# Kernel optimization log

Hardware: AMD Instinct MI355X
Metric: run time of the kernel (lower is better)

The kernel has to match this reference:

```python
import jax, jax.numpy as jnp
import numpy as np

N, CIN, T, V, COUT = 64, 64, 256, 25, 128
CI = COUT // 2  # inter_channels
EPS = 1e-5


def setup_inputs() -> dict:
    key = jax.random.key(0)
    ks = jax.random.split(key, 12)
    s = 0.05
    d = {}
    d['x'] = jax.random.normal(ks[0], (N, CIN, T, V), jnp.float32)
    d['A'] = jax.random.normal(ks[1], (3, V, V), jnp.float32) * s
    d['Al'] = jax.random.normal(ks[2], (3, V, V), jnp.float32) * s
    d['Wp'] = jax.random.normal(ks[3], (3, COUT, CIN), jnp.float32) * s
    d['bp'] = jnp.zeros((3, COUT), jnp.float32)
    d['Wm1'] = jax.random.normal(ks[4], (CI, CIN), jnp.float32) * s
    d['bm1'] = jnp.zeros((CI,), jnp.float32)
    d['Wm2'] = jax.random.normal(ks[5], (CI, CIN), jnp.float32) * s
    d['bm2'] = jnp.zeros((CI,), jnp.float32)
    d['Wm3'] = jax.random.normal(ks[6], (COUT, CI), jnp.float32) * s
    d['bm3'] = jnp.zeros((COUT,), jnp.float32)
    d['Wm4'] = jax.random.normal(ks[7], (COUT, CIN), jnp.float32) * s
    d['bm4'] = jnp.zeros((COUT,), jnp.float32)
    d['alpha'] = jax.random.normal(ks[8], (1,), jnp.float32) * s
    d['bn_gamma'] = jnp.ones((COUT,), jnp.float32)
    d['bn_beta'] = jnp.zeros((COUT,), jnp.float32)
    d['down_W'] = jax.random.normal(ks[9], (COUT, CIN), jnp.float32) * s
    d['down_gamma'] = jnp.ones((COUT,), jnp.float32)
    d['down_beta'] = jnp.zeros((COUT,), jnp.float32)
    return d


def _bn_train(y, gamma, beta):
    # BatchNorm2d training forward: biased batch stats over (N, T, V)
    mu = jnp.mean(y, axis=(0, 2, 3), keepdims=True)
    var = jnp.var(y, axis=(0, 2, 3), keepdims=True)
    return (y - mu) * jax.lax.rsqrt(var + EPS) * gamma[None, :, None, None] + beta[None, :, None, None]


def reference(x, A, Al, Wp, bp, Wm1, bm1, Wm2, bm2, Wm3, bm3, Wm4, bm4,
              alpha, bn_gamma, bn_beta, down_W, down_gamma, down_beta):
    Tn = x.shape[2]
    # --- static graph branch: sum over 3 subsets of (A+Al) graph matmuls ---
    Xp = jnp.einsum('soi,nitv->snotv', Wp, x) + bp[:, None, :, None, None]  # (3,N,COUT,T,V)
    y = jnp.einsum('suv,snctv->nctu', A + Al, Xp)                           # (N,COUT,T,V)
    # --- dynamic adjacency from temporal-difference features ---
    xf = jnp.mean(jnp.einsum('oi,nitv->notv', Wm1, x[:, :, :Tn - 2]) + bm1[None, :, None, None], axis=2)  # (N,CI,V)
    xb = jnp.mean(jnp.einsum('oi,nitv->notv', Wm2, x[:, :, 2:]) + bm2[None, :, None, None], axis=2)       # (N,CI,V)
    diff = xb[:, :, :, None] - xf[:, :, None, :]                            # (N,CI,V,V)
    Rd = jnp.tanh(jnp.einsum('oi,nivw->novw', Wm3, diff) + bm3[None, :, None, None])  # (N,COUT,V,V)
    Xm = jnp.einsum('oi,nitv->notv', Wm4, x) + bm4[None, :, None, None]     # (N,COUT,T,V)
    z = jnp.einsum('ncuv,nctv->nctu', Rd, Xm)                               # (N,COUT,T,V)
    y = z * alpha + y
    # --- BN, residual (1x1 conv + BN down-path since CIN != COUT), ReLU ---
    y = _bn_train(y, bn_gamma, bn_beta)
    d = jnp.einsum('oi,nitv->notv', down_W, x)  # no bias
    d = _bn_train(d, down_gamma, down_beta)
    return jax.nn.relu(y + d)
```

## Files before the change

kernel.cpp:

```cpp
#include <hip/hip_runtime.h>
#include <stdint.h>

typedef unsigned short u16;
typedef unsigned int   u32;
typedef short bf16x8 __attribute__((ext_vector_type(8)));
typedef float f32x4  __attribute__((ext_vector_type(4)));

#define N_    64
#define CIN_  64
#define T_    256
#define V_    25
#define COUT_ 128
#define CI_   64
#define EPS_  1e-5f
#define CNT_  409600.0f

#define MFMA16(a,b,c) __builtin_amdgcn_mfma_f32_16x16x32_bf16((a),(b),(c),0,0,0)

__device__ __forceinline__ u16 f2bf(float f) {
  u32 u = __float_as_uint(f);
  u += 0x7fffu + ((u >> 16) & 1u);
  return (u16)(u >> 16);
}
__device__ __forceinline__ float bf2f(u16 h) { return __uint_as_float(((u32)h) << 16); }

__global__ __launch_bounds__(256) void k_pack(const float* __restrict__ Wp, const float* __restrict__ Wm4,
                                              const float* __restrict__ dW, const float* __restrict__ A,
                                              const float* __restrict__ Al,
                                              u16* __restrict__ w5, u16* __restrict__ bst) {
  int tid = threadIdx.x;
  for (int i = tid; i < 640 * 64; i += 256) {
    int r = i >> 6, k = i & 63;
    float v = (r < 384) ? Wp[i] : (r < 512) ? Wm4[(r - 384) * 64 + k] : dW[(r - 512) * 64 + k];
    w5[i] = f2bf(v);
  }
  for (int i = tid; i < 3 * 32 * 32; i += 256) {
    int s = i >> 10, rem = i & 1023, u = rem >> 5, v = rem & 31;
    float val = (u < 25 && v < 25) ? (A[(s * 25 + u) * 25 + v] + Al[(s * 25 + u) * 25 + v]) : 0.f;
    bst[i] = f2bf(val);
  }
}

__global__ __launch_bounds__(256) void k_means(const float* __restrict__ x,
                                               float* __restrict__ mf, float* __restrict__ mb) {
  int i = blockIdx.x, n = blockIdx.y;
  const float* src = x + ((size_t)n * CIN_ + i) * T_ * V_;
  __shared__ float xs[T_ * V_];
  __shared__ float pf[8][32], pb[8][32];
  for (int idx = threadIdx.x; idx < T_ * V_; idx += 256) xs[idx] = src[idx];
  __syncthreads();
  int v = threadIdx.x & 31, g = threadIdx.x >> 5;
  float sf = 0.f, sb = 0.f;
  if (v < V_) {
    for (int t = g; t < T_; t += 8) {
      float val = xs[t * V_ + v];
      if (t < T_ - 2) sf += val;
      if (t >= 2)     sb += val;
    }
  }
  pf[g][v] = sf; pb[g][v] = sb;
  __syncthreads();
  if (threadIdx.x < V_) {
    float af = 0.f, ab = 0.f;
    for (int gg = 0; gg < 8; gg++) { af += pf[gg][threadIdx.x]; ab += pb[gg][threadIdx.x]; }
    size_t o = ((size_t)n * CIN_ + i) * V_ + threadIdx.x;
    mf[o] = af * (1.0f / 254.0f);
    mb[o] = ab * (1.0f / 254.0f);
  }
}

__global__ __launch_bounds__(256) void k_rd(
    const float* __restrict__ mf, const float* __restrict__ mb,
    const float* __restrict__ Wm1, const float* __restrict__ bm1,
    const float* __restrict__ Wm2, const float* __restrict__ bm2,
    const float* __restrict__ Wm3, const float* __restrict__ bm3,
    const float* __restrict__ bm4, const float* __restrict__ alpha,
    const float* __restrict__ A, const float* __restrict__ Al, const float* __restrict__ bp,
    u16* __restrict__ rdws, float* __restrict__ biasws) {
  int n = blockIdx.x;
  int tid = threadIdx.x;
  __shared__ float MfL[CIN_][V_], MbL[CIN_][V_], xfL[CI_][V_], xbL[CI_][V_];
  __shared__ float PL[COUT_ * V_], QL[COUT_ * V_], rsumL[3][V_];
  for (int idx = tid; idx < CIN_ * V_; idx += 256) {
    MfL[idx / V_][idx % V_] = mf[(size_t)n * CIN_ * V_ + idx];
    MbL[idx / V_][idx % V_] = mb[(size_t)n * CIN_ * V_ + idx];
  }
  if (tid < 75) {
    int s = tid / 25, u = tid % 25;
    float acc = 0.f;
    for (int v = 0; v < 25; v++) acc += A[(s * 25 + u) * 25 + v] + Al[(s * 25 + u) * 25 + v];
    rsumL[s][u] = acc;
  }
  __syncthreads();
  for (int idx = tid; idx < CI_ * V_; idx += 256) {
    int o = idx / V_, v = idx % V_;
    float af = bm1[o], ab = bm2[o];
    for (int i = 0; i < CIN_; i++) {
      af += Wm1[o * CIN_ + i] * MfL[i][v];
      ab += Wm2[o * CIN_ + i] * MbL[i][v];
    }
    xfL[o][v] = af; xbL[o][v] = ab;
  }
  __syncthreads();
  for (int idx = tid; idx < COUT_ * V_; idx += 256) {
    int c = idx / V_, u = idx % V_;
    float p = 0.f, q = 0.f;
    for (int i = 0; i < CI_; i++) {
      p += Wm3[c * CI_ + i] * xbL[i][u];
      q += Wm3[c * CI_ + i] * xfL[i][u];
    }
    PL[idx] = p; QL[idx] = q;
  }
  __syncthreads();
  float al = alpha[0];
  for (int r = tid; r < COUT_ * V_; r += 256) {
    int c = r / V_, u = r % V_;
    float pv = PL[r] + bm3[c];
    float acc = 0.f;
    u16* dst = rdws + ((size_t)(n * COUT_ + c) * 25 + u) * 32;
    for (int w = 0; w < 25; w++) {
      float val = al * tanhf(pv - QL[c * V_ + w]);
      dst[w] = f2bf(val);
      acc += val;
    }
    for (int w = 25; w < 32; w++) dst[w] = 0;
    float yb = 0.f;
    for (int s = 0; s < 3; s++) yb += bp[s * COUT_ + c] * rsumL[s][u];
    biasws[(size_t)(n * COUT_ + c) * 25 + u] = bm4[c] * acc + yb;
  }
}

__global__ __launch_bounds__(256, 2) void k_main(
    const float* __restrict__ x, const u16* __restrict__ w5, const u16* __restrict__ bst,
    const u16* __restrict__ rdws, const float* __restrict__ biasws,
    u16* __restrict__ out16, float* __restrict__ partials) {
  __shared__ __align__(16) char smem[59904];
  __shared__ float statsL[512];
  const int tid = threadIdx.x;
  const int w = tid >> 6, l = tid & 63;
  const int lc = l & 15, lq = l >> 4;
  const int n = blockIdx.y, tc = blockIdx.x, t0 = tc * 16;

  {
    u32* xslw = (u32*)smem;
    const float* xb = x + (size_t)n * CIN_ * T_ * V_ + (size_t)t0 * V_;
    for (int idx = tid; idx < 32 * 416; idx += 256) {
      int i2 = idx / 416, p = idx - i2 * 416;
      float a = 0.f, b = 0.f;
      if (p < 400) {
        a = xb[(size_t)(2 * i2)     * (T_ * V_) + p];
        b = xb[(size_t)(2 * i2 + 1) * (T_ * V_) + p];
      }
      xslw[p * 36 + i2] = ((u32)f2bf(b) << 16) | (u32)f2bf(a);
    }
  }
  bf16x8 bw[3][2];
  #pragma unroll
  for (int s = 0; s < 3; s++)
    #pragma unroll
    for (int ut = 0; ut < 2; ut++)
      bw[s][ut] = *(const bf16x8*)(bst + (s * 32 + ut * 16 + lc) * 32 + lq * 8);
  __syncthreads();

  bf16x8 xf[7][2] = {};
  #pragma unroll
  for (int pi = 0; pi < 7; pi++) {
    int pt = w + pi * 4;
    if (pt < 26) {
      #pragma unroll
      for (int ks = 0; ks < 2; ks++)
        xf[pi][ks] = *(const bf16x8*)((const u16*)smem + (pt * 16 + lc) * 72 + ks * 32 + lq * 8);
    }
  }
  __syncthreads();

  {
    uint4 z4 = {0, 0, 0, 0};
    uint4* q = (uint4*)smem;
    for (int idx = tid; idx < 2304; idx += 256) q[idx] = z4;
    statsL[tid] = 0.f; statsL[tid + 256] = 0.f;
  }
  __syncthreads();

  u16* xpl = (u16*)smem;
  const f32x4 zz = {0.f, 0.f, 0.f, 0.f};

  for (int g = 0; g < 8; g++) {
    const int c0 = g * 16;
    f32x4 acc[4][2];
    #pragma unroll
    for (int cl = 0; cl < 4; cl++) { acc[cl][0] = zz; acc[cl][1] = zz; }
    float ds[4] = {0.f, 0.f, 0.f, 0.f}, dq[4] = {0.f, 0.f, 0.f, 0.f};

    #pragma unroll
    for (int h = 0; h < 2; h++) {
      const int nsl = h ? 3 : 2;
      bf16x8 af[3][2];
      #pragma unroll
      for (int si = 0; si < 3; si++) if (si < nsl) {
        int sl = h * 2 + si;
        #pragma unroll
        for (int ks = 0; ks < 2; ks++)
          af[si][ks] = *(const bf16x8*)(w5 + ((sl * 128 + c0 + lc) * 64 + ks * 32 + lq * 8));
      }
      #pragma unroll
      for (int pi = 0; pi < 7; pi++) {
        int pt = w + pi * 4;
        if (pt >= 26) continue;
        f32x4 pa[3];
        #pragma unroll
        for (int si = 0; si < 3; si++) if (si < nsl) {
          pa[si] = MFMA16(af[si][0], xf[pi][0], zz);
          pa[si] = MFMA16(af[si][1], xf[pi][1], pa[si]);
        }
        int p = pt * 16 + lc;
        if (p < 400) {
          u32 up = (u32)p, t = up / 25u, v = up - t * 25u;
          #pragma unroll
          for (int si = 0; si < 3; si++) if (si < nsl) {
            int sl = h * 2 + si;
            if (sl < 4) {
              int slot = sl & 1;
              u16* dst = xpl + (4 * lq) * 1152 + t * 72 + slot * 32 + v;
              #pragma unroll
              for (int r = 0; r < 4; r++) dst[r * 1152] = f2bf(pa[si][r]);
            } else {
              size_t ob = (((size_t)(n * COUT_ + c0 + 4 * lq) * T_ + t0 + t) * V_ + v) * 2 + 1;
              #pragma unroll
              for (int r = 0; r < 4; r++) {
                float dv = pa[si][r];
                out16[ob + (size_t)r * (T_ * V_ * 2)] = f2bf(dv);
                ds[r] += dv; dq[r] += dv * dv;
              }
            }
          }
        }
      }
      if (h == 1) {
        #pragma unroll
        for (int r = 0; r < 4; r++) {
          float a = ds[r], b = dq[r];
          #pragma unroll
          for (int off = 1; off < 16; off <<= 1) { a += __shfl_xor(a, off); b += __shfl_xor(b, off); }
          if (lc == 0) {
            atomicAdd(&statsL[(c0 + 4 * lq + r) * 4 + 2], a);
            atomicAdd(&statsL[(c0 + 4 * lq + r) * 4 + 3], b);
          }
        }
      }
      __syncthreads();

      {
        bf16x8 rdf0[4], rdf1[4];
        if (h == 1) {
          #pragma unroll
          for (int cl = 0; cl < 4; cl++) {
            size_t rb = (size_t)(n * COUT_ + c0 + w * 4 + cl) * 25;
            rdf0[cl] = *(const bf16x8*)(rdws + (rb + lc) * 32 + lq * 8);
            int u1c = (lc + 16 < 25) ? lc + 16 : 24;
            rdf1[cl] = *(const bf16x8*)(rdws + (rb + u1c) * 32 + lq * 8);
          }
        }
        #pragma unroll
        for (int cl = 0; cl < 4; cl++) {
          int clocal = w * 4 + cl;
          #pragma unroll
          for (int kl = 0; kl < 2; kl++) {
            bf16x8 aX = *(const bf16x8*)(xpl + clocal * 1152 + lc * 72 + kl * 32 + lq * 8);
            int kk = h * 2 + kl;
            bf16x8 b0, b1;
            if (kk < 3) { b0 = bw[kk][0]; b1 = bw[kk][1]; }
            else        { b0 = rdf0[cl];  b1 = rdf1[cl]; }
            acc[cl][0] = MFMA16(aX, b0, acc[cl][0]);
            acc[cl][1] = MFMA16(aX, b1, acc[cl][1]);
          }
        }
      }
      if (h == 1) {
        #pragma unroll
        for (int cl = 0; cl < 4; cl++) {
          int c = c0 + w * 4 + cl;
          size_t bb = (size_t)(n * COUT_ + c) * 25;
          float bias0 = biasws[bb + lc];
          int u1 = lc + 16; bool v1 = u1 < 25;
          float bias1 = biasws[bb + (v1 ? u1 : 24)];
          size_t ob = ((size_t)(n * COUT_ + c) * T_ + t0) * V_;
          float sy = 0.f, sq = 0.f;
          #pragma unroll
          for (int r = 0; r < 4; r++) {
            int t = 4 * lq + r;
            float y0 = acc[cl][0][r] + bias0;
            out16[(ob + t * 25 + lc) * 2] = f2bf(y0);
            sy += y0; sq += y0 * y0;
            float y1 = acc[cl][1][r] + bias1;
            if (v1) {
              out16[(ob + t * 25 + u1) * 2] = f2bf(y1);
              sy += y1; sq += y1 * y1;
            }
          }
          #pragma unroll
          for (int off = 1; off < 64; off <<= 1) { sy += __shfl_xor(sy, off); sq += __shfl_xor(sq, off); }
          if (l == 0) { atomicAdd(&statsL[c * 4 + 0], sy); atomicAdd(&statsL[c * 4 + 1], sq); }
        }
      }
      __syncthreads();
    }
  }
  int bflat = blockIdx.y * 16 + blockIdx.x;
  for (int j = tid; j < 512; j += 256) partials[(size_t)j * 1024 + bflat] = statsL[j];
}

__global__ __launch_bounds__(256) void k_stats1(const float* __restrict__ partials, float* __restrict__ colsum) {
  int w = threadIdx.x >> 6, l = threadIdx.x & 63;
  for (int ci = 0; ci < 8; ci++) {
    int j = blockIdx.x * 32 + w * 8 + ci;
    float s = 0.f;
    for (int it = 0; it < 16; it++) s += partials[(size_t)j * 1024 + it * 64 + l];
    #pragma unroll
    for (int off = 1; off < 64; off <<= 1) s += __shfl_xor(s, off);
    if (l == 0) colsum[j] = s;
  }
}

__global__ __launch_bounds__(128) void k_stats2(
    const float* __restrict__ colsum,
    const float* __restrict__ bn_g, const float* __restrict__ bn_b,
    const float* __restrict__ dn_g, const float* __restrict__ dn_b,
    float* __restrict__ params) {
  int c = threadIdx.x;
  float sy = colsum[c * 4], syy = colsum[c * 4 + 1], sd = colsum[c * 4 + 2], sdd = colsum[c * 4 + 3];
  float muY = sy / CNT_, varY = syy / CNT_ - muY * muY;
  float muD = sd / CNT_, varD = sdd / CNT_ - muD * muD;
  float sY = bn_g[c] * rsqrtf(varY + EPS_);
  float sD = dn_g[c] * rsqrtf(varD + EPS_);
  float off = bn_b[c] - muY * sY + dn_b[c] - muD * sD;
  params[c * 4 + 0] = sY; params[c * 4 + 1] = sD; params[c * 4 + 2] = off;
}

__global__ __launch_bounds__(256) void k_final(u32* __restrict__ io, const float* __restrict__ params) {
  int slab = blockIdx.x;
  int c = slab & (COUT_ - 1);
  float sY = params[c * 4], sD = params[c * 4 + 1], off = params[c * 4 + 2];
  size_t base = (size_t)slab * (T_ * V_);
  #pragma unroll 5
  for (int j = 0; j < 25; j++) {
    size_t idx = base + j * 256 + threadIdx.x;
    u32 w = io[idx];
    float y = bf2f((u16)(w & 0xffffu));
    float d = bf2f((u16)(w >> 16));
    float val = fmaf(y, sY, fmaf(d, sD, off));
    io[idx] = __float_as_uint(fmaxf(val, 0.0f));
  }
}

extern "C" void kernel_launch(void* const* d_in, const int* in_sizes, int n_in,
                              void* d_out, int out_size, void* d_ws, size_t ws_size,
                              hipStream_t stream) {
  const float* x    = (const float*)d_in[0];
  const float* A    = (const float*)d_in[1];
  const float* Al   = (const float*)d_in[2];
  const float* Wp   = (const float*)d_in[3];
  const float* bp   = (const float*)d_in[4];
  const float* Wm1  = (const float*)d_in[5];
  const float* bm1  = (const float*)d_in[6];
  const float* Wm2  = (const float*)d_in[7];
  const float* bm2  = (const float*)d_in[8];
  const float* Wm3  = (const float*)d_in[9];
  const float* bm3  = (const float*)d_in[10];
  const float* Wm4  = (const float*)d_in[11];
  const float* bm4  = (const float*)d_in[12];
  const float* alpha= (const float*)d_in[13];
  const float* bn_g = (const float*)d_in[14];
  const float* bn_b = (const float*)d_in[15];
  const float* dW   = (const float*)d_in[16];
  const float* dn_g = (const float*)d_in[17];
  const float* dn_b = (const float*)d_in[18];

  char* ws = (char*)d_ws;
  float* mf       = (float*)(ws + 0);
  float* mb       = (float*)(ws + 409600);
  u16*   rdws     = (u16*)  (ws + 819200);
  float* biasws   = (float*)(ws + 13926400);
  u16*   w5       = (u16*)  (ws + 14745600);
  u16*   bstw     = (u16*)  (ws + 14827520);
  float* partials = (float*)(ws + 14833664);
  float* colsum   = (float*)(ws + 16930816);
  float* params   = (float*)(ws + 16932864);

  k_pack <<<dim3(1),       dim3(256), 0, stream>>>(Wp, Wm4, dW, A, Al, w5, bstw);
  k_means<<<dim3(64, 64),  dim3(256), 0, stream>>>(x, mf, mb);
  k_rd   <<<dim3(64),      dim3(256), 0, stream>>>(mf, mb, Wm1, bm1, Wm2, bm2, Wm3, bm3,
                                                   bm4, alpha, A, Al, bp, rdws, biasws);
  k_main <<<dim3(16, 64),  dim3(256), 0, stream>>>(x, w5, bstw, rdws, biasws,
                                                   (u16*)d_out, partials);
  k_stats1<<<dim3(16),     dim3(256), 0, stream>>>(partials, colsum);
  k_stats2<<<dim3(1),      dim3(128), 0, stream>>>(colsum, bn_g, bn_b, dn_g, dn_b, params);
  k_final<<<dim3(64 * 128),dim3(256), 0, stream>>>((u32*)d_out, params);
}
```

Baseline: 681.7 us.

## Split Rd kernel for parallelism, shrink main LDS for occupancy, vectorize loads

Splits the per-sample Rd kernel into a projection kernel and a tanh/bias kernel launched over 8x64 blocks, so the costly tanh loop runs across far more blocks. The main kernel stages x in two smaller swizzled LDS halves, which cuts shared memory use and raises launch bounds to 4 blocks per CU. The means and final normalization kernels switch to float4/uint4 vector accesses, and the adjacency row sums move into the pack kernel. Reusing the partials and colsum workspace regions as scratch relies on launch ordering, and the extra sync in the staging loop adds some latency.

Result: slower. 876.6 us (+28.6%).

```diff
diff --git a/kernel.cpp b/kernel.cpp
--- a/kernel.cpp
+++ b/kernel.cpp
@@ -27,7 +27,8 @@
 __global__ __launch_bounds__(256) void k_pack(const float* __restrict__ Wp, const float* __restrict__ Wm4,
                                               const float* __restrict__ dW, const float* __restrict__ A,
                                               const float* __restrict__ Al,
-                                              u16* __restrict__ w5, u16* __restrict__ bst) {
+                                              u16* __restrict__ w5, u16* __restrict__ bst,
+                                              float* __restrict__ rsumw) {
   int tid = threadIdx.x;
   for (int i = tid; i < 640 * 64; i += 256) {
     int r = i >> 6, k = i & 63;
@@ -38,6 +39,12 @@
     int s = i >> 10, rem = i & 1023, u = rem >> 5, v = rem & 31;
     float val = (u < 25 && v < 25) ? (A[(s * 25 + u) * 25 + v] + Al[(s * 25 + u) * 25 + v]) : 0.f;
     bst[i] = f2bf(val);
+  }
+  if (tid < 75) {
+    int s = tid / 25, u = tid % 25;
+    float acc = 0.f;
+    for (int v = 0; v < 25; v++) acc += A[(s * 25 + u) * 25 + v] + Al[(s * 25 + u) * 25 + v];
+    rsumw[tid] = acc;
   }
 }
 
@@ -47,7 +54,11 @@
   const float* src = x + ((size_t)n * CIN_ + i) * T_ * V_;
   __shared__ float xs[T_ * V_];
   __shared__ float pf[8][32], pb[8][32];
-  for (int idx = threadIdx.x; idx < T_ * V_; idx += 256) xs[idx] = src[idx];
+  {
+    float4* xs4 = (float4*)xs;
+    const float4* src4 = (const float4*)src;
+    for (int idx = threadIdx.x; idx < (T_ * V_) / 4; idx += 256) xs4[idx] = src4[idx];
+  }
   __syncthreads();
   int v = threadIdx.x & 31, g = threadIdx.x >> 5;
   float sf = 0.f, sb = 0.f;
@@ -69,27 +80,16 @@
   }
 }
 
-__global__ __launch_bounds__(256) void k_rd(
+__global__ __launch_bounds__(256) void k_rd1(
     const float* __restrict__ mf, const float* __restrict__ mb,
     const float* __restrict__ Wm1, const float* __restrict__ bm1,
     const float* __restrict__ Wm2, const float* __restrict__ bm2,
-    const float* __restrict__ Wm3, const float* __restrict__ bm3,
-    const float* __restrict__ bm4, const float* __restrict__ alpha,
-    const float* __restrict__ A, const float* __restrict__ Al, const float* __restrict__ bp,
-    u16* __restrict__ rdws, float* __restrict__ biasws) {
-  int n = blockIdx.x;
-  int tid = threadIdx.x;
+    const float* __restrict__ Wm3, float* __restrict__ pqws) {
+  int n = blockIdx.x, tid = threadIdx.x;
   __shared__ float MfL[CIN_][V_], MbL[CIN_][V_], xfL[CI_][V_], xbL[CI_][V_];
-  __shared__ float PL[COUT_ * V_], QL[COUT_ * V_], rsumL[3][V_];
   for (int idx = tid; idx < CIN_ * V_; idx += 256) {
     MfL[idx / V_][idx % V_] = mf[(size_t)n * CIN_ * V_ + idx];
     MbL[idx / V_][idx % V_] = mb[(size_t)n * CIN_ * V_ + idx];
-  }
-  if (tid < 75) {
-    int s = tid / 25, u = tid % 25;
-    float acc = 0.f;
-    for (int v = 0; v < 25; v++) acc += A[(s * 25 + u) * 25 + v] + Al[(s * 25 + u) * 25 + v];
-    rsumL[s][u] = acc;
   }
   __syncthreads();
   for (int idx = tid; idx < CI_ * V_; idx += 256) {
@@ -109,70 +109,89 @@
       p += Wm3[c * CI_ + i] * xbL[i][u];
       q += Wm3[c * CI_ + i] * xfL[i][u];
     }
-    PL[idx] = p; QL[idx] = q;
-  }
+    pqws[(size_t)n * 6400 + idx] = p;
+    pqws[(size_t)n * 6400 + 3200 + idx] = q;
+  }
+}
+
+__global__ __launch_bounds__(256) void k_rd2(
+    const float* __restrict__ pqws, const float* __restrict__ rsumw,
+    const float* __restrict__ bm3, const float* __restrict__ bm4,
+    const float* __restrict__ bp, const float* __restrict__ alpha,
+    u16* __restrict__ rdws, float* __restrict__ biasws) {
+  int cg = blockIdx.x, n = blockIdx.y;
+  int c0 = cg * 16, tid = threadIdx.x;
+  __shared__ float Ps[400], Qs[400], rs[75];
+  for (int idx = tid; idx < 400; idx += 256) {
+    Ps[idx] = pqws[(size_t)n * 6400 + c0 * 25 + idx];
+    Qs[idx] = pqws[(size_t)n * 6400 + 3200 + c0 * 25 + idx];
+  }
+  if (tid < 75) rs[tid] = rsumw[tid];
   __syncthreads();
   float al = alpha[0];
-  for (int r = tid; r < COUT_ * V_; r += 256) {
-    int c = r / V_, u = r % V_;
-    float pv = PL[r] + bm3[c];
+  for (int r = tid; r < 400; r += 256) {
+    int cl = r / 25, u = r - cl * 25, c = c0 + cl;
+    float pv = Ps[r] + bm3[c];
     float acc = 0.f;
     u16* dst = rdws + ((size_t)(n * COUT_ + c) * 25 + u) * 32;
-    for (int w = 0; w < 25; w++) {
-      float val = al * tanhf(pv - QL[c * V_ + w]);
-      dst[w] = f2bf(val);
+    for (int w0 = 0; w0 < 25; w0++) {
+      float val = al * tanhf(pv - Qs[cl * 25 + w0]);
+      dst[w0] = f2bf(val);
       acc += val;
     }
-    for (int w = 25; w < 32; w++) dst[w] = 0;
+    for (int w0 = 25; w0 < 32; w0++) dst[w0] = 0;
     float yb = 0.f;
-    for (int s = 0; s < 3; s++) yb += bp[s * COUT_ + c] * rsumL[s][u];
+    for (int s = 0; s < 3; s++) yb += bp[s * COUT_ + c] * rs[s * 25 + u];
     biasws[(size_t)(n * COUT_ + c) * 25 + u] = bm4[c] * acc + yb;
   }
 }
 
-__global__ __launch_bounds__(256, 2) void k_main(
+__global__ __launch_bounds__(256, 4) void k_main(
     const float* __restrict__ x, const u16* __restrict__ w5, const u16* __restrict__ bst,
     const u16* __restrict__ rdws, const float* __restrict__ biasws,
     u16* __restrict__ out16, float* __restrict__ partials) {
-  __shared__ __align__(16) char smem[59904];
+  __shared__ __align__(16) char smem[36864];
   __shared__ float statsL[512];
   const int tid = threadIdx.x;
   const int w = tid >> 6, l = tid & 63;
   const int lc = l & 15, lq = l >> 4;
   const int n = blockIdx.y, tc = blockIdx.x, t0 = tc * 16;
 
-  {
-    u32* xslw = (u32*)smem;
-    const float* xb = x + (size_t)n * CIN_ * T_ * V_ + (size_t)t0 * V_;
-    for (int idx = tid; idx < 32 * 416; idx += 256) {
-      int i2 = idx / 416, p = idx - i2 * 416;
-      float a = 0.f, b = 0.f;
-      if (p < 400) {
-        a = xb[(size_t)(2 * i2)     * (T_ * V_) + p];
-        b = xb[(size_t)(2 * i2 + 1) * (T_ * V_) + p];
-      }
-      xslw[p * 36 + i2] = ((u32)f2bf(b) << 16) | (u32)f2bf(a);
-    }
-  }
   bf16x8 bw[3][2];
   #pragma unroll
   for (int s = 0; s < 3; s++)
     #pragma unroll
     for (int ut = 0; ut < 2; ut++)
       bw[s][ut] = *(const bf16x8*)(bst + (s * 32 + ut * 16 + lc) * 32 + lq * 8);
-  __syncthreads();
 
   bf16x8 xf[7][2] = {};
+  const float* xb = x + (size_t)n * CIN_ * T_ * V_ + (size_t)t0 * V_;
   #pragma unroll
-  for (int pi = 0; pi < 7; pi++) {
-    int pt = w + pi * 4;
-    if (pt < 26) {
-      #pragma unroll
-      for (int ks = 0; ks < 2; ks++)
-        xf[pi][ks] = *(const bf16x8*)((const u16*)smem + (pt * 16 + lc) * 72 + ks * 32 + lq * 8);
-    }
-  }
-  __syncthreads();
+  for (int ks = 0; ks < 2; ks++) {
+    u32* xslw = (u32*)smem;
+    for (int idx = tid; idx < 16 * 416; idx += 256) {
+      int i2 = idx / 416, p = idx - i2 * 416;
+      float a = 0.f, b = 0.f;
+      int ch = ks * 32 + 2 * i2;
+      if (p < 400) {
+        a = xb[(size_t)ch       * (T_ * V_) + p];
+        b = xb[(size_t)(ch + 1) * (T_ * V_) + p];
+      }
+      int f = (p ^ (p >> 2)) & 3;
+      xslw[p * 16 + (i2 ^ (f << 2))] = ((u32)f2bf(b) << 16) | (u32)f2bf(a);
+    }
+    __syncthreads();
+    #pragma unroll
+    for (int pi = 0; pi < 7; pi++) {
+      int pt = w + pi * 4;
+      if (pt < 26) {
+        int p = pt * 16 + lc;
+        int f = (p ^ (p >> 2)) & 3;
+        xf[pi][ks] = *(const bf16x8*)((const u16*)smem + p * 32 + ((lq ^ f) << 3));
+      }
+    }
+    __syncthreads();
+  }
 
   {
     uint4 z4 = {0, 0, 0, 0};
@@ -341,15 +360,19 @@
   int slab = blockIdx.x;
   int c = slab & (COUT_ - 1);
   float sY = params[c * 4], sD = params[c * 4 + 1], off = params[c * 4 + 2];
-  size_t base = (size_t)slab * (T_ * V_);
-  #pragma unroll 5
-  for (int j = 0; j < 25; j++) {
-    size_t idx = base + j * 256 + threadIdx.x;
-    u32 w = io[idx];
-    float y = bf2f((u16)(w & 0xffffu));
-    float d = bf2f((u16)(w >> 16));
-    float val = fmaf(y, sY, fmaf(d, sD, off));
-    io[idx] = __float_as_uint(fmaxf(val, 0.0f));
+  uint4* io4 = (uint4*)io + (size_t)slab * 1600;
+  #pragma unroll
+  for (int j = 0; j < 7; j++) {
+    int idx = j * 256 + (int)threadIdx.x;
+    if (idx < 1600) {
+      uint4 wv = io4[idx];
+      uint4 o;
+      o.x = __float_as_uint(fmaxf(fmaf(bf2f((u16)(wv.x & 0xffffu)), sY, fmaf(bf2f((u16)(wv.x >> 16)), sD, off)), 0.f));
+      o.y = __float_as_uint(fmaxf(fmaf(bf2f((u16)(wv.y & 0xffffu)), sY, fmaf(bf2f((u16)(wv.y >> 16)), sD, off)), 0.f));
+      o.z = __float_as_uint(fmaxf(fmaf(bf2f((u16)(wv.z & 0xffffu)), sY, fmaf(bf2f((u16)(wv.z >> 16)), sD, off)), 0.f));
+      o.w = __float_as_uint(fmaxf(fmaf(bf2f((u16)(wv.w & 0xffffu)), sY, fmaf(bf2f((u16)(wv.w >> 16)), sD, off)), 0.f));
+      io4[idx] = o;
+    }
   }
 }
 
@@ -386,11 +409,13 @@
   float* partials = (float*)(ws + 14833664);
   float* colsum   = (float*)(ws + 16930816);
   float* params   = (float*)(ws + 16932864);
-
-  k_pack <<<dim3(1),       dim3(256), 0, stream>>>(Wp, Wm4, dW, A, Al, w5, bstw);
+  float* pqws  = partials;
+  float* rsumw = colsum;
+
+  k_pack <<<dim3(1),       dim3(256), 0, stream>>>(Wp, Wm4, dW, A, Al, w5, bstw, rsumw);
   k_means<<<dim3(64, 64),  dim3(256), 0, stream>>>(x, mf, mb);
-  k_rd   <<<dim3(64),      dim3(256), 0, stream>>>(mf, mb, Wm1, bm1, Wm2, bm2, Wm3, bm3,
-                                                   bm4, alpha, A, Al, bp, rdws, biasws);
+  k_rd1  <<<dim3(64),      dim3(256), 0, stream>>>(mf, mb, Wm1, bm1, Wm2, bm2, Wm3, pqws);
+  k_rd2  <<<dim3(8, 64),   dim3(256), 0, stream>>>(pqws, rsumw, bm3, bm4, bp, alpha, rdws, biasws);
   k_main <<<dim3(16, 64),  dim3(256), 0, stream>>>(x, w5, bstw, rdws, biasws,
                                                    (u16*)d_out, partials);
   k_stats1<<<dim3(16),     dim3(256), 0, stream>>>(partials, colsum);
```
